# Kernel tuning notes

Measured on AMD Instinct MI355X. Metric: run time of the kernel, lower is better.

## Reference

```python
import jax, jax.numpy as jnp
import numpy as np

DIM = 512
N_HEADS = 8
HEAD_DIM = DIM // N_HEADS
BN_EPS = 1e-5


def setup_inputs() -> dict:
    key = jax.random.key(0)
    ks = jax.random.split(key, 8)
    B, C, H, W = 16, DIM, 32, 32
    x = jax.random.normal(ks[0], (B, C, H, W), dtype=jnp.float32)
    # 1x1 convs == channel matmuls: stacked q/k/v weights [3, out, in], proj [out, in]
    w_qkv = jax.random.normal(ks[1], (3, DIM, DIM), dtype=jnp.float32) * (DIM ** -0.5)
    w_proj = jax.random.normal(ks[2], (DIM, DIM), dtype=jnp.float32) * (DIM ** -0.5)
    # BatchNorm (inference form) params for q/k/v branches, stacked [3, C]
    bn_gamma = jax.random.uniform(ks[3], (3, DIM), minval=0.5, maxval=1.5)
    bn_beta = jax.random.normal(ks[4], (3, DIM)) * 0.1
    bn_mean = jax.random.normal(ks[5], (3, DIM)) * 0.1
    bn_var = jax.random.uniform(ks[6], (3, DIM), minval=0.5, maxval=1.5)
    return {"x": x, "w_qkv": w_qkv, "w_proj": w_proj, "bn_gamma": bn_gamma,
            "bn_beta": bn_beta, "bn_mean": bn_mean, "bn_var": bn_var}


def _ternary_ste(t):
    # forward: sign(t) in {-1,0,1}; backward: identity (straight-through)
    return t + jax.lax.stop_gradient(jnp.sign(t) - t)


def reference(x, w_qkv, w_proj, bn_gamma, bn_beta, bn_mean, bn_var):
    B, C, H, W = x.shape
    N = H * W
    xf = x.reshape(B, C, N)
    # fused 1x1 conv for q,k,v: [3,B,C,N]
    qkv = jnp.einsum('koc,bcn->kbon', w_qkv, xf)
    # BatchNorm (inference): y = (x - mean)/sqrt(var+eps)*gamma + beta
    s = bn_gamma / jnp.sqrt(bn_var + BN_EPS)          # [3,C]
    b = bn_beta - bn_mean * s                          # [3,C]
    qkv = qkv * s[:, None, :, None] + b[:, None, :, None]
    q = _ternary_ste(qkv[0]).reshape(B, N_HEADS, HEAD_DIM, N)
    k = _ternary_ste(qkv[1]).reshape(B, N_HEADS, HEAD_DIM, N)
    v = qkv[2].reshape(B, N_HEADS, HEAD_DIM, N)
    scale = HEAD_DIM ** -0.5
    attn = jnp.einsum('bhdn,bhen->bhde', q, k) * scale  # [B,h,d,d] channel-wise attn
    attn = jax.nn.softmax(attn, axis=-1)
    out = jnp.einsum('bhde,bhen->bhdn', attn, v).reshape(B, C, N)
    out = jnp.einsum('oc,bcn->bon', w_proj, out) + xf   # proj + residual
    return out.reshape(B, C, H, W)
```

## Files before the change

### kernel.cpp

```cpp
#include <hip/hip_runtime.h>
#include <math.h>

#define BN_EPS 1e-5f
#define FIXC 1.0e-4f

typedef _Float16 f16;
typedef _Float16 f16x4 __attribute__((ext_vector_type(4)));
typedef _Float16 f16x8 __attribute__((ext_vector_type(8)));
typedef float f32x4 __attribute__((ext_vector_type(4)));
typedef int i32x4 __attribute__((ext_vector_type(4)));

static constexpr int BB = 16;
static constexpr int C  = 512;
static constexpr int NP = 1024;
static constexpr int NH = 8;
static constexpr int HD = 64;
static constexpr int M3 = 1536;


static constexpr size_t OFF_WHI  = 0;
static constexpr size_t OFF_WLO  = 1572864;
static constexpr size_t OFF_WPH  = 3145728;
static constexpr size_t OFF_SB   = 3670016;
static constexpr size_t OFF_WN   = 3682304;
static constexpr size_t OFF_XN   = 3686400;
static constexpr size_t OFF_FLAG = 3751936;
static constexpr size_t OFF_XTH  = 5849088;
static constexpr size_t OFF_XTL  = 22626304;
static constexpr size_t OFF_AOT  = OFF_XTH;
static constexpr size_t OFF_Q    = 39403520;
static constexpr size_t OFF_K    = 47792128;
static constexpr size_t OFF_VT   = 56180736;

__device__ __forceinline__ void gld16(const void* g, void* l) {
  __builtin_amdgcn_global_load_lds(
      (const __attribute__((address_space(1))) void*)g,
      (__attribute__((address_space(3))) void*)l, 16, 0, 0);
}

__device__ __forceinline__ size_t frag_off(int tile, int kt, int row7, int k5) {
  return (((size_t)tile * 16 + kt) * 8 + (row7 >> 4)) * 512
       + (size_t)((row7 & 15) | ((k5 >> 3) << 4)) * 8;
}

__global__ __launch_bounds__(256) void k_convW(
    const float* __restrict__ wqkv, const float* __restrict__ wproj,
    const float* __restrict__ g, const float* __restrict__ be,
    const float* __restrict__ mu, const float* __restrict__ va,
    f16* __restrict__ Whi, f16* __restrict__ Wlo, f16* __restrict__ Wph,
    float* __restrict__ sA, float* __restrict__ bA, float* __restrict__ wnorm)
{
  const int i = blockIdx.x * 256 + threadIdx.x;
  {
    const int m = i >> 6, l = i & 63;
    const float4 v0 = *(const float4*)&wqkv[(size_t)m * C + l * 8];
    const float4 v1 = *(const float4*)&wqkv[(size_t)m * C + l * 8 + 4];
    const float vv[8] = {v0.x, v0.y, v0.z, v0.w, v1.x, v1.y, v1.z, v1.w};
    f16x8 hv, lv;
    float s2 = 0.f;
#pragma unroll
    for (int q = 0; q < 8; ++q) {
      const f16 h = (f16)vv[q];
      hv[q] = h; lv[q] = (f16)(vv[q] - (float)h);
      s2 = fmaf(vv[q], vv[q], s2);
    }
    *(f16x8*)&Whi[frag_off(m >> 7, l >> 2, m & 127, (l & 3) * 8)] = hv;
    *(f16x8*)&Wlo[(size_t)m * C + l * 8] = lv;
    if (m < 1024) {
      s2 += __shfl_xor(s2, 1);  s2 += __shfl_xor(s2, 2);
      s2 += __shfl_xor(s2, 4);  s2 += __shfl_xor(s2, 8);
      s2 += __shfl_xor(s2, 16); s2 += __shfl_xor(s2, 32);
      if (l == 0) wnorm[m] = sqrtf(s2);
    }
  }
  if (i < 32768) {
    const int m = i >> 6, l = i & 63;
    const float4 v0 = *(const float4*)&wproj[(size_t)m * C + l * 8];
    const float4 v1 = *(const float4*)&wproj[(size_t)m * C + l * 8 + 4];
    const float vv[8] = {v0.x, v0.y, v0.z, v0.w, v1.x, v1.y, v1.z, v1.w};
    f16x8 hv;
#pragma unroll
    for (int q = 0; q < 8; ++q) hv[q] = (f16)vv[q];
    *(f16x8*)&Wph[frag_off(m >> 7, l >> 2, m & 127, (l & 3) * 8)] = hv;
  }
  if (i < M3) {
    const float s = g[i] / sqrtf(va[i] + BN_EPS);
    sA[i] = s;
    bA[i] = be[i] - mu[i] * s;
  }
}

__global__ __launch_bounds__(256) void k_convX(
    const float* __restrict__ x, f16* __restrict__ XtH, f16* __restrict__ XtL,
    float* __restrict__ xnorm2)
{
  const int k0 = blockIdx.x * 64, n0 = blockIdx.y * 64, b = blockIdx.z;
  __shared__ float ls[64][65];
  const int t = threadIdx.x;
  const float* xp = x + ((size_t)b * C + k0) * NP + n0;
  const int c4 = (t & 15) * 4, r0 = t >> 4;
#pragma unroll
  for (int q = 0; q < 4; ++q) {
    const float4 v = *(const float4*)(xp + (size_t)(r0 + q * 16) * NP + c4);
    ls[r0 + q * 16][c4 + 0] = v.x; ls[r0 + q * 16][c4 + 1] = v.y;
    ls[r0 + q * 16][c4 + 2] = v.z; ls[r0 + q * 16][c4 + 3] = v.w;
  }
  __syncthreads();
  if (t < 64) {
    float s2 = 0.f;
#pragma unroll
    for (int q = 0; q < 64; ++q) { const float v = ls[q][t]; s2 = fmaf(v, v, s2); }
    atomicAdd(&xnorm2[(b << 10) + n0 + t], s2);
  }
  const int n = t >> 2, kk = (t & 3) * 16;
  const int n_abs = n0 + n;
  f16x8 hv0 = {}, hv1 = {}, lv0 = {}, lv1 = {};
#pragma unroll
  for (int q = 0; q < 8; ++q) {
    const float v = ls[kk + q][n];
    const f16 h = (f16)v;
    hv0[q] = h; lv0[q] = (f16)(v - (float)h);
  }
#pragma unroll
  for (int q = 0; q < 8; ++q) {
    const float v = ls[kk + 8 + q][n];
    const f16 h = (f16)v;
    hv1[q] = h; lv1[q] = (f16)(v - (float)h);
  }
  const int kb0 = k0 + kk, kb1 = k0 + kk + 8;
  *(f16x8*)&XtH[frag_off(b * 8 + (n_abs >> 7), kb0 >> 5, n_abs & 127, kb0 & 31)] = hv0;
  *(f16x8*)&XtH[frag_off(b * 8 + (n_abs >> 7), kb1 >> 5, n_abs & 127, kb1 & 31)] = hv1;
  *(f16x8*)&XtL[((size_t)b * NP + n_abs) * C + kb0] = lv0;
  *(f16x8*)&XtL[((size_t)b * NP + n_abs) * C + kb1] = lv1;
}

__global__ __launch_bounds__(256, 2) void k_qkv_mfma(
    const f16* __restrict__ Whi, const f16* __restrict__ XtH,
    const float* __restrict__ sA, const float* __restrict__ bA,
    const float* __restrict__ wnorm, const float* __restrict__ xnorm2,
    signed char* __restrict__ qw, signed char* __restrict__ kw,
    f16* __restrict__ vt, unsigned* __restrict__ flagbits)
{
  __shared__ __align__(16) f16 SMEM[8704];

  const int t = threadIdx.x, lane = t & 63, wid = t >> 6;
  const int n0 = blockIdx.x * 128, m0 = blockIdx.y * 128, b = blockIdx.z;

  const f16* Af = Whi + (size_t)(m0 >> 7) * 65536;
  const f16* Bf = XtH + ((size_t)b * 8 + (n0 >> 7)) * 65536;

  f32x4 acc[4][4];
#pragma unroll
  for (int i = 0; i < 4; ++i)
#pragma unroll
    for (int j = 0; j < 4; ++j) acc[i][j] = (f32x4){0.f, 0.f, 0.f, 0.f};

  const int wm = wid >> 1, wn = wid & 1;
  const int lr = lane & 15, ls = lane >> 4;

#define LOADF(KT, AR, BR) do {                                          \
    _Pragma("unroll")                                                   \
    for (int i_ = 0; i_ < 4; ++i_) {                                    \
      (AR)[i_] = *(const f16x8*)&Af[((size_t)(KT) * 8 + wm * 4 + i_) * 512 + lane * 8]; \
      (BR)[i_] = *(const f16x8*)&Bf[((size_t)(KT) * 8 + wn * 4 + i_) * 512 + lane * 8]; \
    }                                                                   \
  } while (0)

#define COMPF(AR, BR) do {                                              \
    _Pragma("unroll")                                                   \
    for (int i_ = 0; i_ < 4; ++i_)                                      \
      _Pragma("unroll")                                                 \
      for (int j_ = 0; j_ < 4; ++j_)                                    \
        acc[i_][j_] = __builtin_amdgcn_mfma_f32_16x16x32_f16(           \
            (AR)[i_], (BR)[j_], acc[i_][j_], 0, 0, 0);                  \
  } while (0)

  {
    f16x8 a0[4], b0[4], a1[4], b1[4];
    LOADF(0, a0, b0);
#pragma unroll
    for (int kt = 0; kt < 16; kt += 2) {
      LOADF(kt + 1, a1, b1);
      COMPF(a0, b0);
      if (kt + 2 < 16) LOADF(kt + 2, a0, b0);
      COMPF(a1, b1);
    }
  }

#undef LOADF
#undef COMPF

  const int kidx = m0 >> 9;
  if (kidx != 2) {
    signed char* dst0 = (kidx == 0) ? qw : kw;
    float xnrm[4];
#pragma unroll
    for (int j = 0; j < 4; ++j)
      xnrm[j] = sqrtf(xnorm2[(b << 10) + n0 + wn * 64 + j * 16 + lr]);
#pragma unroll
    for (int i = 0; i < 4; ++i) {
      float sv[4], bv[4], dl[4];
#pragma unroll
      for (int r = 0; r < 4; ++r) {
        const int o = m0 + wm * 64 + i * 16 + ls * 4 + r;
        sv[r] = sA[o]; bv[r] = bA[o];
        dl[r] = FIXC * wnorm[o] * sv[r];
      }
      const int oc0 = (m0 & 511) + wm * 64 + i * 16 + ls * 4;
      const int og0 = m0 + wm * 64 + i * 16 + ls * 4;
#pragma unroll
      for (int j = 0; j < 4; ++j) {
        const int n = n0 + wn * 64 + j * 16 + lr;
#pragma unroll
        for (int r = 0; r < 4; ++r) {
          const float z = fmaf(acc[i][j][r], sv[r], bv[r]);
          dst0[((size_t)b * C + oc0 + r) * NP + n] =
              (signed char)((z > 0.f) - (z < 0.f));
          if (fabsf(z) <= dl[r] * xnrm[j]) {
            const int of = og0 + r;
            atomicOr(&flagbits[(((size_t)b * NP + n) << 5) + (of >> 5)],
                     1u << (of & 31));
          }
        }
      }
    }
  } else {
    const int c0 = m0 & 511;
    for (int hf = 0; hf < 2; ++hf) {
      __syncthreads();
      if (wn == hf) {
#pragma unroll
        for (int i = 0; i < 4; ++i) {
          float sv[4], bv[4];
#pragma unroll
          for (int r = 0; r < 4; ++r) {
            const int o = m0 + wm * 64 + i * 16 + ls * 4 + r;
            sv[r] = sA[o]; bv[r] = bA[o];
          }
#pragma unroll
          for (int j = 0; j < 4; ++j) {
            f16x4 pk;
#pragma unroll
            for (int r = 0; r < 4; ++r)
              pk[r] = (f16)fmaf(acc[i][j][r], sv[r], bv[r]);
            *(f16x4*)&SMEM[(size_t)(j * 16 + lr) * 136 + wm * 64 + i * 16 + ls * 4] = pk;
          }
        }
      }
      __syncthreads();
      const int nl = t >> 2, cc = (t & 3) * 32;
      const f16* src = &SMEM[(size_t)nl * 136 + cc];
      f16x8 r0 = *(const f16x8*)(src + 0);
      f16x8 r1 = *(const f16x8*)(src + 8);
      f16x8 r2 = *(const f16x8*)(src + 16);
      f16x8 r3 = *(const f16x8*)(src + 24);
      f16* dstv = vt + ((size_t)b * NP + n0 + hf * 64 + nl) * C + c0 + cc;
      *(f16x8*)(dstv + 0)  = r0;
      *(f16x8*)(dstv + 8)  = r1;
      *(f16x8*)(dstv + 16) = r2;
      *(f16x8*)(dstv + 24) = r3;
    }
  }
}

__global__ __launch_bounds__(256) void k_fix(
    const unsigned* __restrict__ flagbits,
    const f16* __restrict__ Whi, const f16* __restrict__ Wlo,
    const f16* __restrict__ XtH, const f16* __restrict__ XtL,
    const float* __restrict__ sA, const float* __restrict__ bA,
    signed char* __restrict__ qw, signed char* __restrict__ kw)
{
  const int wv = blockIdx.x * 4 + (threadIdx.x >> 6);
  const int lane = threadIdx.x & 63;
  const int b = wv >> 10, n = wv & 1023;

  const unsigned* bm = flagbits + ((size_t)wv << 5);
  const unsigned myw = (lane < 32) ? bm[lane] : 0u;
  if (__ballot(myw != 0) == 0ULL) return;

  const int kb = lane * 8;
  const f16x8 bhv = *(const f16x8*)&XtH[
      frag_off(b * 8 + (n >> 7), kb >> 5, n & 127, kb & 31)];
  const f16x8 blv = *(const f16x8*)&XtL[((size_t)b * NP + n) * C + kb];
  float xv[8];
#pragma unroll
  for (int q = 0; q < 8; ++q) xv[q] = (float)bhv[q] + (float)blv[q];

  for (int w = 0; w < 32; ++w) {
    unsigned bits = __shfl(myw, w);
    while (bits) {
      const int o = w * 32 + __builtin_ctz(bits);
      bits &= bits - 1;
      const f16x8 ahv = *(const f16x8*)&Whi[
          frag_off(o >> 7, kb >> 5, o & 127, kb & 31)];
      const f16x8 alv = *(const f16x8*)&Wlo[(size_t)o * C + kb];
      float s = 0.f;
#pragma unroll
      for (int q = 0; q < 8; ++q)
        s = fmaf((float)ahv[q] + (float)alv[q], xv[q], s);
      s += __shfl_xor(s, 1);  s += __shfl_xor(s, 2);  s += __shfl_xor(s, 4);
      s += __shfl_xor(s, 8);  s += __shfl_xor(s, 16); s += __shfl_xor(s, 32);
      if (lane == 0) {
        const float y = fmaf(s, sA[o], bA[o]);
        const signed char sg = (signed char)((y > 0.f) - (y < 0.f));
        if (o < 512) qw[((size_t)b * C + o) * NP + n] = sg;
        else         kw[((size_t)b * C + (o - 512)) * NP + n] = sg;
      }
    }
  }
}

__global__ __launch_bounds__(256) void k_attn_fused(
    const signed char* __restrict__ qw, const signed char* __restrict__ kw,
    const f16* __restrict__ vt, f16* __restrict__ aot)
{
  const int half = blockIdx.x;
  const int bh = blockIdx.y;
  const int b = bh >> 3, h = bh & 7;
  const int t = threadIdx.x, lane = t & 63, wid = t >> 6;
  const int dw = wid * 16;
  const int lr = lane & 15, lg = lane >> 4;

  __shared__ f16 ph[64][72];
  __shared__ f16 pl[64][72];
  __shared__ f16 sb[64][72];

  const signed char* qp = qw + ((size_t)b * C + h * HD + dw + lr) * NP;
  const signed char* kp = kw + ((size_t)b * C + h * HD + lr) * NP;

  i32x4 accS[4];
#pragma unroll
  for (int j = 0; j < 4; ++j) accS[j] = (i32x4){0, 0, 0, 0};

#pragma unroll 4
  for (int ks = 0; ks < 16; ++ks) {
    const i32x4 af = *(const i32x4*)(qp + ks * 64 + lg * 16);
#pragma unroll
    for (int j = 0; j < 4; ++j) {
      const i32x4 bf = *(const i32x4*)(kp + (size_t)(j * 16) * NP + ks * 64 + lg * 16);
      accS[j] = __builtin_amdgcn_mfma_i32_16x16x64_i8(af, bf, accS[j], 0, 0, 0);
    }
  }

#pragma unroll
  for (int r = 0; r < 4; ++r) {
    float mx = (float)accS[0][r];
#pragma unroll
    for (int j = 1; j < 4; ++j) mx = fmaxf(mx, (float)accS[j][r]);
    mx = fmaxf(mx, __shfl_xor(mx, 1));
    mx = fmaxf(mx, __shfl_xor(mx, 2));
    mx = fmaxf(mx, __shfl_xor(mx, 4));
    mx = fmaxf(mx, __shfl_xor(mx, 8));
    float pvv[4];
    float sm = 0.f;
#pragma unroll
    for (int j = 0; j < 4; ++j) {
      pvv[j] = expf(((float)accS[j][r] - mx) * 0.125f);
      sm += pvv[j];
    }
    sm += __shfl_xor(sm, 1);
    sm += __shfl_xor(sm, 2);
    sm += __shfl_xor(sm, 4);
    sm += __shfl_xor(sm, 8);
    const float inv = 1.f / sm;
    const int drow = dw + lg * 4 + r;
#pragma unroll
    for (int j = 0; j < 4; ++j) {
      const float p = pvv[j] * inv;
      const f16 hi = (f16)p;
      ph[drow][j * 16 + lr] = hi;
      pl[drow][j * 16 + lr] = (f16)(p - (float)hi);
    }
  }
  __syncthreads();

  const f16x8 pa0h = *(const f16x8*)&ph[dw + lr][lg * 8];
  const f16x8 pa0l = *(const f16x8*)&pl[dw + lr][lg * 8];
  const f16x8 pa1h = *(const f16x8*)&ph[dw + lr][32 + lg * 8];
  const f16x8 pa1l = *(const f16x8*)&pl[dw + lr][32 + lg * 8];

  const f16* vbase = vt + (size_t)b * NP * C + h * HD;
  const int nbase = half * 512;

  for (int nc = 0; nc < 8; ++nc) {
    const int nn0 = nbase + nc * 64;
    __syncthreads();
#pragma unroll
    for (int nt = 0; nt < 4; ++nt) {
      const f16* vp = vbase + (size_t)(nn0 + nt * 16 + lr) * C + lg * 8;
      const f16x8 bv0 = *(const f16x8*)(vp);
      const f16x8 bv1 = *(const f16x8*)(vp + 32);
      f32x4 acc = (f32x4){0.f, 0.f, 0.f, 0.f};
      acc = __builtin_amdgcn_mfma_f32_16x16x32_f16(pa0h, bv0, acc, 0, 0, 0);
      acc = __builtin_amdgcn_mfma_f32_16x16x32_f16(pa0l, bv0, acc, 0, 0, 0);
      acc = __builtin_amdgcn_mfma_f32_16x16x32_f16(pa1h, bv1, acc, 0, 0, 0);
      acc = __builtin_amdgcn_mfma_f32_16x16x32_f16(pa1l, bv1, acc, 0, 0, 0);
      f16x4 pk;
#pragma unroll
      for (int r = 0; r < 4; ++r) pk[r] = (f16)acc[r];
      *(f16x4*)&sb[nt * 16 + lr][dw + lg * 4] = pk;
    }
    __syncthreads();
    const int nl = t >> 2, cc = (t & 3) * 16;
    const f16x8 o0 = *(const f16x8*)&sb[nl][cc];
    const f16x8 o1 = *(const f16x8*)&sb[nl][cc + 8];
    const int n_abs = nn0 + nl;
    const int c1 = h * HD + cc, c2 = h * HD + cc + 8;
    *(f16x8*)&aot[frag_off(b * 8 + (n_abs >> 7), c1 >> 5, n_abs & 127, c1 & 31)] = o0;
    *(f16x8*)&aot[frag_off(b * 8 + (n_abs >> 7), c2 >> 5, n_abs & 127, c2 & 31)] = o1;
  }
}

__global__ __launch_bounds__(256) void k_proj_mfma(
    const f16* __restrict__ Wph, const f16* __restrict__ aot,
    const float* __restrict__ X, float* __restrict__ out)
{
  __shared__ __align__(16) f16 SMEM[32768];
  f16* const As0 = SMEM;
  f16* const Bs0 = SMEM + 8192;
  f16* const As1 = SMEM + 16384;
  f16* const Bs1 = SMEM + 24576;

  const int t = threadIdx.x, lane = t & 63, wid = t >> 6;
  const int n0 = blockIdx.x * 128, m0 = blockIdx.y * 128, b = blockIdx.z;

  const f16* Af = Wph + (size_t)(m0 >> 7) * 65536;
  const f16* Bf = aot + ((size_t)b * 8 + (n0 >> 7)) * 65536;

  f32x4 acc[4][4];
#pragma unroll
  for (int i = 0; i < 4; ++i)
#pragma unroll
    for (int j = 0; j < 4; ++j) acc[i][j] = (f32x4){0.f, 0.f, 0.f, 0.f};

  const int wm = wid >> 1, wn = wid & 1;
  const int lr = lane & 15, ls = lane >> 4;
  const int soff = wid * 512 + lane * 8;

#define PSTAGE(TI, AS, BS) do {                                         \
    const f16* Ak_ = Af + (size_t)(TI) * 8192;                          \
    const f16* Bk_ = Bf + (size_t)(TI) * 8192;                          \
    _Pragma("unroll")                                                   \
    for (int r_ = 0; r_ < 4; ++r_) {                                    \
      gld16(Ak_ + r_ * 2048 + soff, &(AS)[r_ * 2048 + wid * 512]);      \
      gld16(Bk_ + r_ * 2048 + soff, &(BS)[r_ * 2048 + wid * 512]);      \
    }                                                                   \
  } while (0)

#define PCOMP(AS, BS) do {                                              \
    _Pragma("unroll")                                                   \
    for (int ksub_ = 0; ksub_ < 2; ++ksub_) {                           \
      f16x8 ah_[4], bh_[4];                                             \
      _Pragma("unroll")                                                 \
      for (int i_ = 0; i_ < 4; ++i_) {                                  \
        ah_[i_] = *(const f16x8*)&(AS)[ksub_ * 4096 + (wm * 4 + i_) * 512 + lane * 8]; \
        bh_[i_] = *(const f16x8*)&(BS)[ksub_ * 4096 + (wn * 4 + i_) * 512 + lane * 8]; \
      }                                                                 \
      _Pragma("unroll")                                                 \
      for (int i_ = 0; i_ < 4; ++i_)                                    \
        _Pragma("unroll")                                               \
        for (int j_ = 0; j_ < 4; ++j_)                                  \
          acc[i_][j_] = __builtin_amdgcn_mfma_f32_16x16x32_f16(         \
              ah_[i_], bh_[j_], acc[i_][j_], 0, 0, 0);                  \
    }                                                                   \
  } while (0)

  PSTAGE(0, As0, Bs0);
#pragma unroll
  for (int ti = 0; ti < 8; ++ti) {
    if (ti < 7) {
      if (ti & 1) PSTAGE(ti + 1, As0, Bs0);
      else        PSTAGE(ti + 1, As1, Bs1);
      asm volatile("s_waitcnt vmcnt(8)" ::: "memory");
    } else {
      asm volatile("s_waitcnt vmcnt(0)" ::: "memory");
    }
    __builtin_amdgcn_sched_barrier(0);
    __builtin_amdgcn_s_barrier();
    if (ti & 1) PCOMP(As1, Bs1); else PCOMP(As0, Bs0);
    asm volatile("s_waitcnt lgkmcnt(0)" ::: "memory");
    __builtin_amdgcn_sched_barrier(0);
    __builtin_amdgcn_s_barrier();
  }

#undef PSTAGE
#undef PCOMP

#pragma unroll
  for (int i = 0; i < 4; ++i) {
    const int oc0 = m0 + wm * 64 + i * 16 + ls * 4;
#pragma unroll
    for (int j = 0; j < 4; ++j) {
      const int n = n0 + wn * 64 + j * 16 + lr;
#pragma unroll
      for (int r = 0; r < 4; ++r) {
        const size_t idx = ((size_t)b * C + oc0 + r) * NP + n;
        out[idx] = acc[i][j][r] + X[idx];
      }
    }
  }
}

extern "C" void kernel_launch(void* const* d_in, const int* in_sizes, int n_in,
                              void* d_out, int out_size, void* d_ws, size_t ws_size,
                              hipStream_t stream)
{
  const float* x      = (const float*)d_in[0];
  const float* w_qkv  = (const float*)d_in[1];
  const float* w_proj = (const float*)d_in[2];
  const float* g      = (const float*)d_in[3];
  const float* be     = (const float*)d_in[4];
  const float* mu     = (const float*)d_in[5];
  const float* va     = (const float*)d_in[6];
  float* out = (float*)d_out;

  char* ws = (char*)d_ws;
  f16*  Whi = (f16*)(ws + OFF_WHI);
  f16*  Wlo = (f16*)(ws + OFF_WLO);
  f16*  Wph = (f16*)(ws + OFF_WPH);
  float* sA = (float*)(ws + OFF_SB);
  float* bA = sA + M3;
  float* wn = (float*)(ws + OFF_WN);
  float* xn2 = (float*)(ws + OFF_XN);
  unsigned* flagbits = (unsigned*)(ws + OFF_FLAG);
  f16*  XtH = (f16*)(ws + OFF_XTH);
  f16*  XtL = (f16*)(ws + OFF_XTL);
  f16*  aot = (f16*)(ws + OFF_AOT);
  signed char* qw = (signed char*)(ws + OFF_Q);
  signed char* kw = (signed char*)(ws + OFF_K);
  f16*  vtw = (f16*)(ws + OFF_VT);

  hipMemsetAsync(xn2, 0, OFF_XTH - OFF_XN, stream);

  k_convW<<<dim3(384), 256, 0, stream>>>(
      w_qkv, w_proj, g, be, mu, va, Whi, Wlo, Wph, sA, bA, wn);
  k_convX<<<dim3(C / 64, NP / 64, BB), 256, 0, stream>>>(x, XtH, XtL, xn2);
  k_qkv_mfma<<<dim3(NP / 128, M3 / 128, BB), 256, 0, stream>>>(
      Whi, XtH, sA, bA, wn, xn2, qw, kw, vtw, flagbits);
  k_fix<<<dim3(BB * NP / 4), 256, 0, stream>>>(
      flagbits, Whi, Wlo, XtH, XtL, sA, bA, qw, kw);
  k_attn_fused<<<dim3(2, BB * NH), 256, 0, stream>>>(qw, kw, vtw, aot);
  k_proj_mfma<<<dim3(NP / 128, C / 128, BB), 256, 0, stream>>>(Wph, aot, x, out);
}
```

Baseline: 139.3 us.

## Stage QKV GEMM operands through LDS with 4-deep direct-to-LDS pipeline

The QKV MFMA kernel previously loaded A/B fragments straight from global memory into registers with double buffering. It now issues direct global-to-LDS loads (gld16) into a 4-slot ring buffer three tiles ahead, waits on vmcnt counters, and reads fragments from LDS for the MFMAs. LDS usage grows to 64KB and the occupancy hint of 2 blocks per CU is dropped, which lowers occupancy and adds two barriers per k-tile.

```diff
diff --git a/kernel.cpp b/kernel.cpp
--- a/kernel.cpp
+++ b/kernel.cpp
@@ -134,14 +134,14 @@
   *(f16x8*)&XtL[((size_t)b * NP + n_abs) * C + kb1] = lv1;
 }
 
-__global__ __launch_bounds__(256, 2) void k_qkv_mfma(
+__global__ __launch_bounds__(256) void k_qkv_mfma(
     const f16* __restrict__ Whi, const f16* __restrict__ XtH,
     const float* __restrict__ sA, const float* __restrict__ bA,
     const float* __restrict__ wnorm, const float* __restrict__ xnorm2,
     signed char* __restrict__ qw, signed char* __restrict__ kw,
     f16* __restrict__ vt, unsigned* __restrict__ flagbits)
 {
-  __shared__ __align__(16) f16 SMEM[8704];
+  __shared__ __align__(16) f16 SMEM[32768];
 
   const int t = threadIdx.x, lane = t & 63, wid = t >> 6;
   const int n0 = blockIdx.x * 128, m0 = blockIdx.y * 128, b = blockIdx.z;
@@ -157,38 +157,51 @@
 
   const int wm = wid >> 1, wn = wid & 1;
   const int lr = lane & 15, ls = lane >> 4;
-
-#define LOADF(KT, AR, BR) do {                                          \
+  const int soff = wid * 512 + lane * 8;
+
+#define QSTAGE(TI, K) do {                                              \
+    const f16* Ak_ = Af + (size_t)(TI) * 4096;                          \
+    const f16* Bk_ = Bf + (size_t)(TI) * 4096;                          \
+    _Pragma("unroll")                                                   \
+    for (int r_ = 0; r_ < 2; ++r_) {                                    \
+      gld16(Ak_ + r_ * 2048 + soff, &SMEM[(K) * 8192 + r_ * 2048 + wid * 512]); \
+      gld16(Bk_ + r_ * 2048 + soff, &SMEM[(K) * 8192 + 4096 + r_ * 2048 + wid * 512]); \
+    }                                                                   \
+  } while (0)
+
+#define QCOMP(K) do {                                                   \
+    f16x8 ah_[4], bh_[4];                                               \
     _Pragma("unroll")                                                   \
     for (int i_ = 0; i_ < 4; ++i_) {                                    \
-      (AR)[i_] = *(const f16x8*)&Af[((size_t)(KT) * 8 + wm * 4 + i_) * 512 + lane * 8]; \
-      (BR)[i_] = *(const f16x8*)&Bf[((size_t)(KT) * 8 + wn * 4 + i_) * 512 + lane * 8]; \
+      ah_[i_] = *(const f16x8*)&SMEM[(K) * 8192 + (wm * 4 + i_) * 512 + lane * 8]; \
+      bh_[i_] = *(const f16x8*)&SMEM[(K) * 8192 + 4096 + (wn * 4 + i_) * 512 + lane * 8]; \
     }                                                                   \
-  } while (0)
-
-#define COMPF(AR, BR) do {                                              \
     _Pragma("unroll")                                                   \
     for (int i_ = 0; i_ < 4; ++i_)                                      \
       _Pragma("unroll")                                                 \
       for (int j_ = 0; j_ < 4; ++j_)                                    \
         acc[i_][j_] = __builtin_amdgcn_mfma_f32_16x16x32_f16(           \
-            (AR)[i_], (BR)[j_], acc[i_][j_], 0, 0, 0);                  \
+            ah_[i_], bh_[j_], acc[i_][j_], 0, 0, 0);                    \
   } while (0)
 
-  {
-    f16x8 a0[4], b0[4], a1[4], b1[4];
-    LOADF(0, a0, b0);
-#pragma unroll
-    for (int kt = 0; kt < 16; kt += 2) {
-      LOADF(kt + 1, a1, b1);
-      COMPF(a0, b0);
-      if (kt + 2 < 16) LOADF(kt + 2, a0, b0);
-      COMPF(a1, b1);
-    }
-  }
-
-#undef LOADF
-#undef COMPF
+  QSTAGE(0, 0); QSTAGE(1, 1); QSTAGE(2, 2);
+#pragma unroll
+  for (int ti = 0; ti < 16; ++ti) {
+    if (ti + 3 < 16) QSTAGE(ti + 3, (ti + 3) & 3);
+    if (ti <= 12)      asm volatile("s_waitcnt vmcnt(12)" ::: "memory");
+    else if (ti == 13) asm volatile("s_waitcnt vmcnt(8)"  ::: "memory");
+    else if (ti == 14) asm volatile("s_waitcnt vmcnt(4)"  ::: "memory");
+    else               asm volatile("s_waitcnt vmcnt(0)"  ::: "memory");
+    __builtin_amdgcn_sched_barrier(0);
+    __builtin_amdgcn_s_barrier();
+    QCOMP(ti & 3);
+    asm volatile("s_waitcnt lgkmcnt(0)" ::: "memory");
+    __builtin_amdgcn_sched_barrier(0);
+    __builtin_amdgcn_s_barrier();
+  }
+
+#undef QSTAGE
+#undef QCOMP
 
   const int kidx = m0 >> 9;
   if (kidx != 2) {
```

Measured after the change: 134.8 us. 3.3% less time.

## Stage B tiles through LDS with double-buffered async loads in QKV GEMM

Applied to the files above, without the earlier changes.

The QKV MFMA kernel now stages the shared X fragment tiles (B operand) into LDS with direct global-to-LDS loads, double-buffered across k-steps of 64, while A fragments stay in registers. Each wave reads B from LDS instead of loading it from global memory itself, which cuts redundant global traffic between the two wm wave pairs. Explicit waitcnt and barrier control overlaps the next tile's loads with the current compute. LDS grows to 32 KB and launch bounds rise to 3 blocks per CU, which may increase register pressure and adds two barriers per iteration.

```diff
diff --git a/kernel.cpp b/kernel.cpp
--- a/kernel.cpp
+++ b/kernel.cpp
@@ -134,14 +134,14 @@
   *(f16x8*)&XtL[((size_t)b * NP + n_abs) * C + kb1] = lv1;
 }
 
-__global__ __launch_bounds__(256, 2) void k_qkv_mfma(
+__global__ __launch_bounds__(256, 3) void k_qkv_mfma(
     const f16* __restrict__ Whi, const f16* __restrict__ XtH,
     const float* __restrict__ sA, const float* __restrict__ bA,
     const float* __restrict__ wnorm, const float* __restrict__ xnorm2,
     signed char* __restrict__ qw, signed char* __restrict__ kw,
     f16* __restrict__ vt, unsigned* __restrict__ flagbits)
 {
-  __shared__ __align__(16) f16 SMEM[8704];
+  __shared__ __align__(16) f16 SMEM[16384];
 
   const int t = threadIdx.x, lane = t & 63, wid = t >> 6;
   const int n0 = blockIdx.x * 128, m0 = blockIdx.y * 128, b = blockIdx.z;
@@ -158,37 +158,62 @@
   const int wm = wid >> 1, wn = wid & 1;
   const int lr = lane & 15, ls = lane >> 4;
 
-#define LOADF(KT, AR, BR) do {                                          \
+#define ALOAD(TI, AR) do {                                              \
     _Pragma("unroll")                                                   \
-    for (int i_ = 0; i_ < 4; ++i_) {                                    \
-      (AR)[i_] = *(const f16x8*)&Af[((size_t)(KT) * 8 + wm * 4 + i_) * 512 + lane * 8]; \
-      (BR)[i_] = *(const f16x8*)&Bf[((size_t)(KT) * 8 + wn * 4 + i_) * 512 + lane * 8]; \
+    for (int u_ = 0; u_ < 8; ++u_)                                      \
+      (AR)[u_] = *(const f16x8*)&Af[(size_t)(TI) * 8192 +               \
+          ((u_ >> 2) * 8 + wm * 4 + (u_ & 3)) * 512 + lane * 8];        \
+  } while (0)
+
+#define BSTAGE(TI, K) do {                                              \
+    const f16* Bk_ = Bf + (size_t)(TI) * 8192;                          \
+    _Pragma("unroll")                                                   \
+    for (int r_ = 0; r_ < 4; ++r_)                                      \
+      gld16(Bk_ + r_ * 2048 + t * 8, &SMEM[(K) * 8192 + r_ * 2048 + wid * 512]); \
+  } while (0)
+
+#define QCOMP(AR, K) do {                                               \
+    _Pragma("unroll")                                                   \
+    for (int ksub_ = 0; ksub_ < 2; ++ksub_) {                           \
+      f16x8 bh_[4];                                                     \
+      _Pragma("unroll")                                                 \
+      for (int j_ = 0; j_ < 4; ++j_)                                    \
+        bh_[j_] = *(const f16x8*)&SMEM[(K) * 8192 + ksub_ * 4096 +      \
+            (wn * 4 + j_) * 512 + lane * 8];                            \
+      _Pragma("unroll")                                                 \
+      for (int i_ = 0; i_ < 4; ++i_)                                    \
+        _Pragma("unroll")                                               \
+        for (int j_ = 0; j_ < 4; ++j_)                                  \
+          acc[i_][j_] = __builtin_amdgcn_mfma_f32_16x16x32_f16(         \
+              (AR)[ksub_ * 4 + i_], bh_[j_], acc[i_][j_], 0, 0, 0);     \
     }                                                                   \
   } while (0)
 
-#define COMPF(AR, BR) do {                                              \
-    _Pragma("unroll")                                                   \
-    for (int i_ = 0; i_ < 4; ++i_)                                      \
-      _Pragma("unroll")                                                 \
-      for (int j_ = 0; j_ < 4; ++j_)                                    \
-        acc[i_][j_] = __builtin_amdgcn_mfma_f32_16x16x32_f16(           \
-            (AR)[i_], (BR)[j_], acc[i_][j_], 0, 0, 0);                  \
-  } while (0)
-
   {
-    f16x8 a0[4], b0[4], a1[4], b1[4];
-    LOADF(0, a0, b0);
-#pragma unroll
-    for (int kt = 0; kt < 16; kt += 2) {
-      LOADF(kt + 1, a1, b1);
-      COMPF(a0, b0);
-      if (kt + 2 < 16) LOADF(kt + 2, a0, b0);
-      COMPF(a1, b1);
-    }
-  }
-
-#undef LOADF
-#undef COMPF
+    f16x8 a0[8], a1[8];
+    ALOAD(0, a0);
+    BSTAGE(0, 0);
+#pragma unroll
+    for (int ti = 0; ti < 8; ++ti) {
+      if (ti < 7) {
+        if (ti & 1) { ALOAD(ti + 1, a0); BSTAGE(ti + 1, 0); }
+        else        { ALOAD(ti + 1, a1); BSTAGE(ti + 1, 1); }
+        asm volatile("s_waitcnt vmcnt(12)" ::: "memory");
+      } else {
+        asm volatile("s_waitcnt vmcnt(0)" ::: "memory");
+      }
+      __builtin_amdgcn_sched_barrier(0);
+      __builtin_amdgcn_s_barrier();
+      if (ti & 1) QCOMP(a1, 1); else QCOMP(a0, 0);
+      asm volatile("s_waitcnt lgkmcnt(0)" ::: "memory");
+      __builtin_amdgcn_sched_barrier(0);
+      __builtin_amdgcn_s_barrier();
+    }
+  }
+
+#undef ALOAD
+#undef BSTAGE
+#undef QCOMP
 
   const int kidx = m0 >> 9;
   if (kidx != 2) {
```

Result: faster. 134.2 us (-3.7%).
